# Kernel optimization log

Measured on AMD Instinct MI355X. Metric: run time of the kernel, lower is better.

The kernel has to match this reference:

```python
import jax, jax.numpy as jnp
import numpy as np

N = 100000        # nodes
E = 1600000       # edges (avg degree 16)
F = 128           # num_features
H = 8             # heads
D = F // H        # head_dim


def setup_inputs() -> dict:
    key = jax.random.key(0)
    ks = jax.random.split(key, 11)
    s = 1.0 / np.sqrt(F)
    return {
        "feat": jax.random.normal(ks[0], (N, F), dtype=jnp.float32),
        "edge_src": jax.random.randint(ks[1], (E,), 0, N, dtype=jnp.int32),
        "edge_dst": jax.random.randint(ks[2], (E,), 0, N, dtype=jnp.int32),
        "Wq": jax.random.uniform(ks[3], (F, F), jnp.float32, -s, s),
        "bq": jax.random.uniform(ks[4], (F,), jnp.float32, -s, s),
        "Wk": jax.random.uniform(ks[5], (F, F), jnp.float32, -s, s),
        "bk": jax.random.uniform(ks[6], (F,), jnp.float32, -s, s),
        "Wv": jax.random.uniform(ks[7], (F, F), jnp.float32, -s, s),
        "bv": jax.random.uniform(ks[8], (F,), jnp.float32, -s, s),
        "Wo": jax.random.uniform(ks[9], (F, F), jnp.float32, -s, s),
        "bo": jax.random.uniform(ks[10], (F,), jnp.float32, -s, s),
    }


def reference(feat, edge_src, edge_dst, Wq, bq, Wk, bk, Wv, bv, Wo, bo):
    scale = D ** -0.5
    # projections, split into heads: [N, H, D]
    q = ((feat @ Wq.T + bq) * scale).reshape(N, H, D)
    k = (feat @ Wk.T + bk).reshape(N, H, D)
    v = (feat @ Wv.T + bv).reshape(N, H, D)

    # per-edge dot product k[src] . q[dst] -> [E, H]  (dfn.u_dot_v)
    scores = jnp.einsum('ehd,ehd->eh', k[edge_src], q[edge_dst])

    # edge softmax normalized over incoming edges of each dst node
    m = jax.ops.segment_max(scores, edge_dst, num_segments=N)  # [N, H]
    m = jnp.where(jnp.isfinite(m), m, 0.0)
    e = jnp.exp(scores - m[edge_dst])                          # [E, H]
    z = jax.ops.segment_sum(e, edge_dst, num_segments=N)       # [N, H]
    alpha = e / z[edge_dst]                                    # [E, H]

    # weighted sum aggregation (u_mul_e + sum): [N, H, D]
    wv = alpha[:, :, None] * v[edge_src]                       # [E, H, D]
    attn = jax.ops.segment_sum(wv, edge_dst, num_segments=N)

    return attn.reshape(N, F) @ Wo.T + bo
```

## Files before the change

kernel.cpp:

```cpp
#include <hip/hip_runtime.h>
#include <math.h>

#define N_NODES 100000
#define N_EDGES 1600000
#define FDIM 128
#define NHEAD 8
#define HDIM 16
#define NBUK 391
#define NPART 400
#define PCHUNK 4000

using bf16x8 = __attribute__((ext_vector_type(8))) short;
using half8  = __attribute__((ext_vector_type(8))) _Float16;
using f32x4  = __attribute__((ext_vector_type(4))) float;
using f32x2  = __attribute__((ext_vector_type(2))) float;

__device__ inline unsigned short f2bf(float f) {
    union { float f; unsigned int u; } x; x.f = f;
    unsigned int u = x.u;
    return (unsigned short)((u + 0x7fffu + ((u >> 16) & 1u)) >> 16);
}
__device__ inline unsigned short f2h(float f) {
    _Float16 h = (_Float16)f;
    return __builtin_bit_cast(unsigned short, h);
}
__device__ inline unsigned int packh2(float a, float b) {
    return (unsigned int)f2h(a) | ((unsigned int)f2h(b) << 16);
}
__device__ inline float h_lo(unsigned int u) {
    return (float)__builtin_bit_cast(_Float16, (unsigned short)(u & 0xffffu));
}
__device__ inline float h_hi(unsigned int u) {
    return (float)__builtin_bit_cast(_Float16, (unsigned short)(u >> 16));
}
__device__ inline float exp2_fast(float x) {
#if __has_builtin(__builtin_amdgcn_exp2f)
    return __builtin_amdgcn_exp2f(x);
#else
    return __expf(x * 0.6931471805599453f);
#endif
}

#if __has_builtin(__builtin_amdgcn_cvt_pk_fp8_f32)
__device__ inline unsigned char fp8_enc(float x) {
    return (unsigned char)(__builtin_amdgcn_cvt_pk_fp8_f32(x, x, 0, false) & 0xff);
}
#else
__device__ inline unsigned char fp8_enc(float x) {
    unsigned int u = __builtin_bit_cast(unsigned int, x);
    unsigned int s = (u >> 24) & 0x80;
    float ax = fabsf(x);
    if (!(ax >= 0.001953125f)) {
        int m = (int)(ax * 512.f + 0.5f);
        return (unsigned char)(s | (unsigned)(m > 7 ? 7 : m));
    }
    if (ax > 448.f) return (unsigned char)(s | 0x7e);
    int e; float fr = frexpf(ax, &e);
    int q = (int)(fr * 16.f + 0.5f);
    if (q == 16) { q = 8; e += 1; }
    int exp = e - 1 + 7;
    if (exp <= 0) { int m = (int)(ax * 512.f + 0.5f); return (unsigned char)(s | (unsigned)(m > 7 ? 7 : m)); }
    if (exp > 15) return (unsigned char)(s | 0x7e);
    return (unsigned char)(s | (exp << 3) | (q & 7));
}
#endif

#if __has_builtin(__builtin_amdgcn_cvt_pk_f32_fp8)
#define FP8_HW_DECODE 1
#else
__device__ inline float fp8_dec_sw(unsigned char b) {
    int s = b >> 7, e = (b >> 3) & 15, m = b & 7;
    float v = (e == 0) ? ldexpf((float)m, -9) : ldexpf((float)(8 + m), e - 10);
    return s ? -v : v;
}
#endif

__device__ inline float dot_fp8_16(uint4 kr, const f32x2* __restrict__ qq2) {
#ifdef FP8_HW_DECODE
    f32x2 a = {0.f, 0.f};
    f32x2 p;
    p = __builtin_amdgcn_cvt_pk_f32_fp8(kr.x, false); a += p * qq2[0];
    p = __builtin_amdgcn_cvt_pk_f32_fp8(kr.x, true);  a += p * qq2[1];
    p = __builtin_amdgcn_cvt_pk_f32_fp8(kr.y, false); a += p * qq2[2];
    p = __builtin_amdgcn_cvt_pk_f32_fp8(kr.y, true);  a += p * qq2[3];
    p = __builtin_amdgcn_cvt_pk_f32_fp8(kr.z, false); a += p * qq2[4];
    p = __builtin_amdgcn_cvt_pk_f32_fp8(kr.z, true);  a += p * qq2[5];
    p = __builtin_amdgcn_cvt_pk_f32_fp8(kr.w, false); a += p * qq2[6];
    p = __builtin_amdgcn_cvt_pk_f32_fp8(kr.w, true);  a += p * qq2[7];
    return a[0] + a[1];
#else
    const float* qq = (const float*)qq2;
    float s = 0.f;
    unsigned int wds[4] = {kr.x, kr.y, kr.z, kr.w};
#pragma unroll
    for (int i = 0; i < 4; ++i)
#pragma unroll
        for (int j = 0; j < 4; ++j)
            s = fmaf(fp8_dec_sw((wds[i] >> (8 * j)) & 0xff), qq[i * 4 + j], s);
    return s;
#endif
}

__global__ __launch_bounds__(256) void convert_w_kernel(
    const float* __restrict__ W0, const float* __restrict__ W1,
    const float* __restrict__ W2, const float* __restrict__ W3,
    unsigned short* __restrict__ out)
{
    int i = blockIdx.x * 256 + threadIdx.x;
    int j  = i & 7;
    int l  = (i >> 3) & 63;
    int fk = i >> 9;
    int ks = fk & 3, nf = fk >> 2;
    int s = (nf * 16 + (l & 15)) * FDIM + ks * 32 + (l >> 4) * 8 + j;
    out[i]             = f2bf(W0[s]);
    out[16384 + i]     = f2bf(W1[s]);
    out[2 * 16384 + i] = f2bf(W2[s]);
    out[3 * 16384 + i] = f2h(W3[s]);
}

__global__ __launch_bounds__(256) void csr_hist_kernel(
    const int* __restrict__ edst, int* __restrict__ cntmatT)
{
    __shared__ int hist[NBUK];
    for (int b = threadIdx.x; b < NBUK; b += 256) hist[b] = 0;
    __syncthreads();
    const int c0 = blockIdx.x * PCHUNK;
    const int ce = min(c0 + PCHUNK, N_EDGES);
    for (int i = c0 + threadIdx.x; i < ce; i += 256) {
        int d = __builtin_nontemporal_load(&edst[i]);
        atomicAdd(&hist[d >> 8], 1);
    }
    __syncthreads();
    for (int b = threadIdx.x; b < NBUK; b += 256)
        cntmatT[b * NPART + blockIdx.x] = hist[b];
}

__global__ __launch_bounds__(512) void csr_colscan_kernel(
    const int* __restrict__ cntmatT, int* __restrict__ preT, int* __restrict__ colsum)
{
    __shared__ int s[512];
    const int t = threadIdx.x, buk = blockIdx.x;
    int x = (t < NPART) ? cntmatT[buk * NPART + t] : 0;
    s[t] = x;
    __syncthreads();
    for (int off = 1; off < 512; off <<= 1) {
        int v = (t >= off) ? s[t - off] : 0;
        __syncthreads();
        s[t] += v;
        __syncthreads();
    }
    if (t < NPART) preT[buk * NPART + t] = s[t] - x;
    if (t == NPART - 1) colsum[buk] = s[t];
}

__global__ __launch_bounds__(512) void csr_basescan_kernel(
    const int* __restrict__ colsum, int* __restrict__ base, int* __restrict__ row_off)
{
    __shared__ int s[512];
    const int t = threadIdx.x;
    int x = (t < NBUK) ? colsum[t] : 0;
    s[t] = x;
    __syncthreads();
    for (int off = 1; off < 512; off <<= 1) {
        int v = (t >= off) ? s[t - off] : 0;
        __syncthreads();
        s[t] += v;
        __syncthreads();
    }
    if (t < NBUK) base[t] = s[t] - x;
    if (t == 0) { base[NBUK] = N_EDGES; row_off[N_NODES] = N_EDGES; }
}

__global__ __launch_bounds__(256) void csr_partition_kernel(
    const int* __restrict__ esrc, const int* __restrict__ edst,
    const int* __restrict__ preT, const int* __restrict__ base,
    uint2* __restrict__ bpair)
{
    __shared__ int cur[NBUK];
    for (int b = threadIdx.x; b < NBUK; b += 256)
        cur[b] = base[b] + preT[b * NPART + blockIdx.x];
    __syncthreads();
    const int c0 = blockIdx.x * PCHUNK;
    const int ce = min(c0 + PCHUNK, N_EDGES);
    for (int i = c0 + threadIdx.x; i < ce; i += 256) {
        int d = __builtin_nontemporal_load(&edst[i]);
        int s = __builtin_nontemporal_load(&esrc[i]);
        int slot = atomicAdd(&cur[d >> 8], 1);
        bpair[slot] = make_uint2((unsigned)s, (unsigned)d);
    }
}

__global__ __launch_bounds__(256) void csr_bucket_kernel(
    const uint2* __restrict__ bpair, const int* __restrict__ base,
    int* __restrict__ row_off, int* __restrict__ csr_src)
{
    __shared__ int cnt2[256], s[256], cur[256];
    const int buk = blockIdx.x, t = threadIdx.x;
    const int b0 = base[buk];
    const int sz = base[buk + 1] - b0;
    const int nb0 = buk << 8;

    cnt2[t] = 0;
    __syncthreads();
    for (int i = t; i < sz; i += 256)
        atomicAdd(&cnt2[bpair[b0 + i].y & 255u], 1);
    __syncthreads();

    int x = cnt2[t];
    s[t] = x;
    __syncthreads();
    for (int off = 1; off < 256; off <<= 1) {
        int v = (t >= off) ? s[t - off] : 0;
        __syncthreads();
        s[t] += v;
        __syncthreads();
    }
    int excl = s[t] - x;
    cur[t] = excl;
    if (nb0 + t < N_NODES) row_off[nb0 + t] = b0 + excl;
    __syncthreads();

    for (int i = t; i < sz; i += 256) {
        uint2 p = bpair[b0 + i];
        int r = atomicAdd(&cur[p.y & 255u], 1);
        csr_src[b0 + r] = (int)p.x;
    }
}

struct GemmArgs {
    const unsigned short* W[3];
    const float* b[3];
    void* out[3];
    float scale[3];
};

template<int NP, bool IN_F32, bool MFMA_F16, int OUTM>
__global__ __launch_bounds__(256, 2) void mfma_gemm_v2(
    const void* __restrict__ Ain, GemmArgs ga, int nrows)
{
    __shared__ unsigned short A_s[128][136];
    __shared__ unsigned short W_sh[8192];

    const int t  = threadIdx.x;
    const int r0 = blockIdx.x * 128;

#pragma unroll
    for (int it = 0; it < 8; ++it) {
        int i = t + it * 256;
        int r = i >> 4, c8 = (i & 15) << 3;
        int gr = r0 + r;
        if (IN_F32) {
            float4 v0 = make_float4(0.f, 0.f, 0.f, 0.f), v1 = v0;
            if (gr < nrows) {
                const float* Af = (const float*)Ain;
                v0 = *(const float4*)&Af[(size_t)gr * FDIM + c8];
                v1 = *(const float4*)&Af[(size_t)gr * FDIM + c8 + 4];
            }
            uint4 pk;
            pk.x = (unsigned)f2bf(v0.x) | ((unsigned)f2bf(v0.y) << 16);
            pk.y = (unsigned)f2bf(v0.z) | ((unsigned)f2bf(v0.w) << 16);
            pk.z = (unsigned)f2bf(v1.x) | ((unsigned)f2bf(v1.y) << 16);
            pk.w = (unsigned)f2bf(v1.z) | ((unsigned)f2bf(v1.w) << 16);
            *(uint4*)&A_s[r][c8] = pk;
        } else {
            uint4 v = make_uint4(0u, 0u, 0u, 0u);
            if (gr < nrows) {
                const unsigned short* Ab = (const unsigned short*)Ain;
                v = *(const uint4*)&Ab[(size_t)gr * FDIM + c8];
            }
            *(uint4*)&A_s[r][c8] = v;
        }
    }
    __syncthreads();

    const int w  = t >> 6, l = t & 63;
    const int lr = l & 15, lk = l >> 4;

    bf16x8 a[2][4];
#pragma unroll
    for (int rg = 0; rg < 2; ++rg)
#pragma unroll
        for (int ks = 0; ks < 4; ++ks)
            a[rg][ks] = *(const bf16x8*)&A_s[w * 32 + rg * 16 + lr][ks * 32 + lk * 8];

#pragma unroll
    for (int p = 0; p < NP; ++p) {
        const unsigned short* Wsrc = ga.W[p];
        f32x4 acc[2][8];
#pragma unroll
        for (int rg = 0; rg < 2; ++rg)
#pragma unroll
            for (int nf = 0; nf < 8; ++nf) acc[rg][nf] = (f32x4){0.f, 0.f, 0.f, 0.f};

#pragma unroll
        for (int h = 0; h < 2; ++h) {
#pragma unroll
            for (int it = 0; it < 4; ++it) {
                int chunk = t + it * 256;
                *(uint4*)&W_sh[chunk * 8] = *(const uint4*)&Wsrc[h * 8192 + chunk * 8];
            }
            __syncthreads();
#pragma unroll
            for (int nfl = 0; nfl < 4; ++nfl) {
                int nf = h * 4 + nfl;
#pragma unroll
                for (int ks = 0; ks < 4; ++ks) {
                    bf16x8 bfr = *(const bf16x8*)&W_sh[((nfl * 4 + ks) * 64 + l) * 8];
                    if (MFMA_F16) {
                        acc[0][nf] = __builtin_amdgcn_mfma_f32_16x16x32_f16(
                            __builtin_bit_cast(half8, a[0][ks]), __builtin_bit_cast(half8, bfr),
                            acc[0][nf], 0, 0, 0);
                        acc[1][nf] = __builtin_amdgcn_mfma_f32_16x16x32_f16(
                            __builtin_bit_cast(half8, a[1][ks]), __builtin_bit_cast(half8, bfr),
                            acc[1][nf], 0, 0, 0);
                    } else {
                        acc[0][nf] = __builtin_amdgcn_mfma_f32_16x16x32_bf16(a[0][ks], bfr, acc[0][nf], 0, 0, 0);
                        acc[1][nf] = __builtin_amdgcn_mfma_f32_16x16x32_bf16(a[1][ks], bfr, acc[1][nf], 0, 0, 0);
                    }
                }
            }
            __syncthreads();
        }

        const float* bias = ga.b[p];
        const float  scl  = ga.scale[p];
        const int    mode = (OUTM >> (2 * p)) & 3;

        if (mode == 0) {
            unsigned short* Oh = &A_s[0][0];
#pragma unroll
            for (int rg = 0; rg < 2; ++rg)
#pragma unroll
                for (int nf = 0; nf < 8; ++nf) {
                    int col = nf * 16 + lr;
                    float bv = bias[col];
#pragma unroll
                    for (int j = 0; j < 4; ++j)
                        Oh[(w * 32 + rg * 16 + lk * 4 + j) * 136 + col] = f2h((acc[rg][nf][j] + bv) * scl);
                }
            __syncthreads();
            unsigned short* outp = (unsigned short*)ga.out[p];
#pragma unroll
            for (int it = 0; it < 8; ++it) {
                int i = t + it * 256;
                int r = i >> 4, c8 = (i & 15) << 3;
                if (r0 + r < nrows)
                    *(uint4*)&outp[(size_t)(r0 + r) * FDIM + c8] = *(const uint4*)&Oh[r * 136 + c8];
            }
        } else if (mode == 1) {
            unsigned char* O8 = (unsigned char*)A_s;
#pragma unroll
            for (int rg = 0; rg < 2; ++rg)
#pragma unroll
                for (int nf = 0; nf < 8; ++nf) {
                    int col = nf * 16 + lr;
                    float bv = bias[col];
#pragma unroll
                    for (int j = 0; j < 4; ++j)
                        O8[(w * 32 + rg * 16 + lk * 4 + j) * 144 + col] = fp8_enc((acc[rg][nf][j] + bv) * scl);
                }
            __syncthreads();
            unsigned char* outp = (unsigned char*)ga.out[p];
#pragma unroll
            for (int it = 0; it < 4; ++it) {
                int i = t + it * 256;
                int r = i >> 3, c16 = (i & 7) << 4;
                if (r0 + r < nrows)
                    *(uint4*)&outp[(size_t)(r0 + r) * FDIM + c16] = *(const uint4*)&O8[r * 144 + c16];
            }
        } else {
            float* outp = (float*)ga.out[p];
#pragma unroll
            for (int rg = 0; rg < 2; ++rg)
#pragma unroll
                for (int nf = 0; nf < 8; ++nf) {
                    int col = nf * 16 + lr;
                    float bv = bias[col];
                    int row = r0 + w * 32 + rg * 16 + lk * 4;
#pragma unroll
                    for (int j = 0; j < 4; ++j)
                        if (row + j < nrows)
                            outp[(size_t)(row + j) * FDIM + col] = (acc[rg][nf][j] + bv) * scl;
                }
        }
    }
}

__global__ __launch_bounds__(256) void attn_kernel(
    const unsigned short* __restrict__ q, const unsigned char* __restrict__ kf8,
    const unsigned short* __restrict__ v,
    const int* __restrict__ row_off, const int* __restrict__ csr_src,
    unsigned short* __restrict__ out, int nnodes)
{
    __shared__ float q_s[4][NHEAD][18];
    __shared__ float p_s[4][64][NHEAD];
    __shared__ int   src_s[4][64];

    const int w = threadIdx.x >> 6;
    const int l = threadIdx.x & 63;
    const int node = blockIdx.x * 4 + w;
    if (node >= nnodes) return;

    {
        unsigned int qv = *(const unsigned int*)&q[(size_t)node * FDIM + l * 2];
        *(f32x2*)&q_s[w][l >> 3][(l & 7) * 2] = (f32x2){h_lo(qv), h_hi(qv)};
    }

    const int e_l = l >> 3, h_sc = l & 7;
    const int e2 = l >> 4, h_ag = (l >> 1) & 7, dq = l & 1;
    const int vo = h_ag * HDIM + dq * 8;

    const int start = row_off[node];
    const int end   = row_off[node + 1];

    float z_run = 0.f;
    f32x2 acc[4] = {{0.f,0.f},{0.f,0.f},{0.f,0.f},{0.f,0.f}};

    const f32x2* qq2 = (const f32x2*)&q_s[w][h_sc][0];

    for (int c0 = start; c0 < end; c0 += 64) {
        const int cn = min(64, end - c0);

        for (int i = l; i < cn; i += 64)
            src_s[w][i] = csr_src[c0 + i];

        for (int base = 0; base < cn; base += 32) {
            uint4 kr[4];
#pragma unroll
            for (int it = 0; it < 4; ++it) {
                int ei = base + it * 8 + e_l;
                if (ei < cn)
                    kr[it] = *(const uint4*)&kf8[(size_t)src_s[w][ei] * FDIM + h_sc * 16];
            }
#pragma unroll
            for (int it = 0; it < 4; ++it) {
                int ei = base + it * 8 + e_l;
                if (ei < cn) {
                    float p = exp2_fast(dot_fp8_16(kr[it], qq2));
                    p_s[w][ei][h_sc] = p;
                    z_run += p;
                }
            }
        }

        for (int base = 0; base < cn; base += 4) {
            int e  = base + e2;
            int ec = min(e, cn - 1);
            float p = (e < cn) ? p_s[w][e][h_ag] : 0.f;
            uint4 vv = *(const uint4*)&v[(size_t)src_s[w][ec] * FDIM + vo];
            f32x2 p2 = {p, p};
            acc[0] += p2 * (f32x2){h_lo(vv.x), h_hi(vv.x)};
            acc[1] += p2 * (f32x2){h_lo(vv.y), h_hi(vv.y)};
            acc[2] += p2 * (f32x2){h_lo(vv.z), h_hi(vv.z)};
            acc[3] += p2 * (f32x2){h_lo(vv.w), h_hi(vv.w)};
        }
    }

#pragma unroll
    for (int mask = 8; mask < 64; mask <<= 1)
        z_run += __shfl_xor(z_run, mask, 64);

#pragma unroll
    for (int mask = 16; mask < 64; mask <<= 1)
#pragma unroll
        for (int i = 0; i < 4; ++i) {
            acc[i][0] += __shfl_xor(acc[i][0], mask, 64);
            acc[i][1] += __shfl_xor(acc[i][1], mask, 64);
        }

    float z_ag = __shfl(z_run, h_ag, 64);

    if (e2 == 0) {
        uint4 o = make_uint4(0u, 0u, 0u, 0u);
        if (end > start) {
            float rz = 1.0f / z_ag;
            o.x = packh2(acc[0][0] * rz, acc[0][1] * rz);
            o.y = packh2(acc[1][0] * rz, acc[1][1] * rz);
            o.z = packh2(acc[2][0] * rz, acc[2][1] * rz);
            o.w = packh2(acc[3][0] * rz, acc[3][1] * rz);
        }
        *(uint4*)&out[(size_t)node * FDIM + vo] = o;
    }
}

extern "C" void kernel_launch(void* const* d_in, const int* in_sizes, int n_in,
                              void* d_out, int out_size, void* d_ws, size_t ws_size,
                              hipStream_t stream)
{
    const float* feat = (const float*)d_in[0];
    const int*   esrc = (const int*)d_in[1];
    const int*   edst = (const int*)d_in[2];
    const float* Wq   = (const float*)d_in[3];
    const float* bq   = (const float*)d_in[4];
    const float* Wk   = (const float*)d_in[5];
    const float* bk   = (const float*)d_in[6];
    const float* Wv   = (const float*)d_in[7];
    const float* bv   = (const float*)d_in[8];
    const float* Wo   = (const float*)d_in[9];
    const float* bo   = (const float*)d_in[10];
    float* out = (float*)d_out;

    const size_t NROW = (size_t)N_NODES * FDIM;
    unsigned short* qb  = (unsigned short*)d_ws;
    unsigned short* vb  = qb + NROW;
    unsigned short* ab  = vb + NROW;
    unsigned char*  kf8 = (unsigned char*)(ab + NROW);
    unsigned short* wbf = (unsigned short*)(kf8 + NROW);
    int* cntmatT = (int*)(wbf + 4 * 16384);
    int* preT    = cntmatT + NBUK * NPART;
    int* colsum  = preT + NBUK * NPART;
    int* base    = colsum + 512;
    uint2* bpair = (uint2*)(base + 512);
    int* row_off = (int*)(bpair + N_EDGES);
    int* csr_src = row_off + N_NODES + 1;

    const int gemmGrid = (N_NODES + 127) / 128;

    hipLaunchKernelGGL(convert_w_kernel, dim3(64), dim3(256), 0, stream,
                       Wq, Wk, Wv, Wo, wbf);

    GemmArgs qkv;
    qkv.W[0] = wbf;          qkv.b[0] = bq; qkv.out[0] = qb;  qkv.scale[0] = 0.25f * 1.4426950408889634f;
    qkv.W[1] = wbf + 16384;  qkv.b[1] = bk; qkv.out[1] = kf8; qkv.scale[1] = 1.0f;
    qkv.W[2] = wbf + 32768;  qkv.b[2] = bv; qkv.out[2] = vb;  qkv.scale[2] = 1.0f;
    hipLaunchKernelGGL((mfma_gemm_v2<3, true, false, 4>), dim3(gemmGrid), dim3(256), 0, stream,
                       feat, qkv, N_NODES);

    hipLaunchKernelGGL(csr_hist_kernel, dim3(NPART), dim3(256), 0, stream, edst, cntmatT);
    hipLaunchKernelGGL(csr_colscan_kernel, dim3(NBUK), dim3(512), 0, stream, cntmatT, preT, colsum);
    hipLaunchKernelGGL(csr_basescan_kernel, dim3(1), dim3(512), 0, stream, colsum, base, row_off);
    hipLaunchKernelGGL(csr_partition_kernel, dim3(NPART), dim3(256), 0, stream,
                       esrc, edst, preT, base, bpair);
    hipLaunchKernelGGL(csr_bucket_kernel, dim3(NBUK), dim3(256), 0, stream,
                       bpair, base, row_off, csr_src);

    hipLaunchKernelGGL(attn_kernel, dim3((N_NODES + 3) / 4), dim3(256), 0, stream,
                       qb, kf8, vb, row_off, csr_src, ab, N_NODES);

    GemmArgs oprj;
    oprj.W[0] = wbf + 3 * 16384; oprj.b[0] = bo; oprj.out[0] = out; oprj.scale[0] = 1.0f;
    hipLaunchKernelGGL((mfma_gemm_v2<1, false, true, 2>), dim3(gemmGrid), dim3(256), 0, stream,
                       ab, oprj, N_NODES);
}
```

Before: 222.7 us.

## Merge CSR build kernels with weight conversion and QKV GEMM launches

Fuses weight conversion with the destination histogram into one launch, merges the column scan and base scan using a last-block-done atomic counter, and runs the QKV projection GEMM blocks alongside the edge partition blocks in a single heterogeneous grid. This cuts the kernel launch count from eight to five and lets the independent GEMM and partition work share the GPU at the same time instead of running back to back. The cost is larger register and shared-memory footprints for the partition blocks, which now share the GEMM's launch bounds. It also adds reliance on a device-scope counter reset inside the first kernel.

```diff
diff --git a/kernel.cpp b/kernel.cpp
--- a/kernel.cpp
+++ b/kernel.cpp
@@ -101,30 +101,31 @@
 #endif
 }
 
-__global__ __launch_bounds__(256) void convert_w_kernel(
+__global__ __launch_bounds__(256) void convert_hist_kernel(
     const float* __restrict__ W0, const float* __restrict__ W1,
     const float* __restrict__ W2, const float* __restrict__ W3,
-    unsigned short* __restrict__ out)
-{
-    int i = blockIdx.x * 256 + threadIdx.x;
-    int j  = i & 7;
-    int l  = (i >> 3) & 63;
-    int fk = i >> 9;
-    int ks = fk & 3, nf = fk >> 2;
-    int s = (nf * 16 + (l & 15)) * FDIM + ks * 32 + (l >> 4) * 8 + j;
-    out[i]             = f2bf(W0[s]);
-    out[16384 + i]     = f2bf(W1[s]);
-    out[2 * 16384 + i] = f2bf(W2[s]);
-    out[3 * 16384 + i] = f2h(W3[s]);
-}
-
-__global__ __launch_bounds__(256) void csr_hist_kernel(
-    const int* __restrict__ edst, int* __restrict__ cntmatT)
+    unsigned short* __restrict__ out,
+    const int* __restrict__ edst, int* __restrict__ cntmatT, int* __restrict__ done)
 {
     __shared__ int hist[NBUK];
+    if (blockIdx.x < 64) {
+        int i = blockIdx.x * 256 + threadIdx.x;
+        if (i == 0) done[0] = 0;
+        int j  = i & 7;
+        int l  = (i >> 3) & 63;
+        int fk = i >> 9;
+        int ks = fk & 3, nf = fk >> 2;
+        int s = (nf * 16 + (l & 15)) * FDIM + ks * 32 + (l >> 4) * 8 + j;
+        out[i]             = f2bf(W0[s]);
+        out[16384 + i]     = f2bf(W1[s]);
+        out[2 * 16384 + i] = f2bf(W2[s]);
+        out[3 * 16384 + i] = f2h(W3[s]);
+        return;
+    }
+    const int pb = blockIdx.x - 64;
     for (int b = threadIdx.x; b < NBUK; b += 256) hist[b] = 0;
     __syncthreads();
-    const int c0 = blockIdx.x * PCHUNK;
+    const int c0 = pb * PCHUNK;
     const int ce = min(c0 + PCHUNK, N_EDGES);
     for (int i = c0 + threadIdx.x; i < ce; i += 256) {
         int d = __builtin_nontemporal_load(&edst[i]);
@@ -132,13 +133,15 @@
     }
     __syncthreads();
     for (int b = threadIdx.x; b < NBUK; b += 256)
-        cntmatT[b * NPART + blockIdx.x] = hist[b];
-}
-
-__global__ __launch_bounds__(512) void csr_colscan_kernel(
-    const int* __restrict__ cntmatT, int* __restrict__ preT, int* __restrict__ colsum)
+        cntmatT[b * NPART + pb] = hist[b];
+}
+
+__global__ __launch_bounds__(512) void csr_scan_kernel(
+    const int* __restrict__ cntmatT, int* __restrict__ preT, int* __restrict__ colsum,
+    int* __restrict__ base, int* __restrict__ row_off, int* __restrict__ done)
 {
     __shared__ int s[512];
+    __shared__ int isLast;
     const int t = threadIdx.x, buk = blockIdx.x;
     int x = (t < NPART) ? cntmatT[buk * NPART + t] : 0;
     s[t] = x;
@@ -150,16 +153,17 @@
         __syncthreads();
     }
     if (t < NPART) preT[buk * NPART + t] = s[t] - x;
-    if (t == NPART - 1) colsum[buk] = s[t];
-}
-
-__global__ __launch_bounds__(512) void csr_basescan_kernel(
-    const int* __restrict__ colsum, int* __restrict__ base, int* __restrict__ row_off)
-{
-    __shared__ int s[512];
-    const int t = threadIdx.x;
-    int x = (t < NBUK) ? colsum[t] : 0;
-    s[t] = x;
+    if (t == NPART - 1)
+        __hip_atomic_store(&colsum[buk], s[t], __ATOMIC_RELAXED, __HIP_MEMORY_SCOPE_AGENT);
+    __threadfence();
+    __syncthreads();
+    if (t == 0)
+        isLast = (atomicAdd(done, 1) == NBUK - 1) ? 1 : 0;
+    __syncthreads();
+    if (!isLast) return;
+    __threadfence();
+    int y = (t < NBUK) ? __hip_atomic_load(&colsum[t], __ATOMIC_RELAXED, __HIP_MEMORY_SCOPE_AGENT) : 0;
+    s[t] = y;
     __syncthreads();
     for (int off = 1; off < 512; off <<= 1) {
         int v = (t >= off) ? s[t - off] : 0;
@@ -167,64 +171,8 @@
         s[t] += v;
         __syncthreads();
     }
-    if (t < NBUK) base[t] = s[t] - x;
+    if (t < NBUK) base[t] = s[t] - y;
     if (t == 0) { base[NBUK] = N_EDGES; row_off[N_NODES] = N_EDGES; }
-}
-
-__global__ __launch_bounds__(256) void csr_partition_kernel(
-    const int* __restrict__ esrc, const int* __restrict__ edst,
-    const int* __restrict__ preT, const int* __restrict__ base,
-    uint2* __restrict__ bpair)
-{
-    __shared__ int cur[NBUK];
-    for (int b = threadIdx.x; b < NBUK; b += 256)
-        cur[b] = base[b] + preT[b * NPART + blockIdx.x];
-    __syncthreads();
-    const int c0 = blockIdx.x * PCHUNK;
-    const int ce = min(c0 + PCHUNK, N_EDGES);
-    for (int i = c0 + threadIdx.x; i < ce; i += 256) {
-        int d = __builtin_nontemporal_load(&edst[i]);
-        int s = __builtin_nontemporal_load(&esrc[i]);
-        int slot = atomicAdd(&cur[d >> 8], 1);
-        bpair[slot] = make_uint2((unsigned)s, (unsigned)d);
-    }
-}
-
-__global__ __launch_bounds__(256) void csr_bucket_kernel(
-    const uint2* __restrict__ bpair, const int* __restrict__ base,
-    int* __restrict__ row_off, int* __restrict__ csr_src)
-{
-    __shared__ int cnt2[256], s[256], cur[256];
-    const int buk = blockIdx.x, t = threadIdx.x;
-    const int b0 = base[buk];
-    const int sz = base[buk + 1] - b0;
-    const int nb0 = buk << 8;
-
-    cnt2[t] = 0;
-    __syncthreads();
-    for (int i = t; i < sz; i += 256)
-        atomicAdd(&cnt2[bpair[b0 + i].y & 255u], 1);
-    __syncthreads();
-
-    int x = cnt2[t];
-    s[t] = x;
-    __syncthreads();
-    for (int off = 1; off < 256; off <<= 1) {
-        int v = (t >= off) ? s[t - off] : 0;
-        __syncthreads();
-        s[t] += v;
-        __syncthreads();
-    }
-    int excl = s[t] - x;
-    cur[t] = excl;
-    if (nb0 + t < N_NODES) row_off[nb0 + t] = b0 + excl;
-    __syncthreads();
-
-    for (int i = t; i < sz; i += 256) {
-        uint2 p = bpair[b0 + i];
-        int r = atomicAdd(&cur[p.y & 255u], 1);
-        csr_src[b0 + r] = (int)p.x;
-    }
 }
 
 struct GemmArgs {
@@ -235,14 +183,14 @@
 };
 
 template<int NP, bool IN_F32, bool MFMA_F16, int OUTM>
-__global__ __launch_bounds__(256, 2) void mfma_gemm_v2(
-    const void* __restrict__ Ain, GemmArgs ga, int nrows)
+__device__ __forceinline__ void gemm_body(const void* __restrict__ Ain,
+                                          const GemmArgs& ga, int nrows, int blk)
 {
     __shared__ unsigned short A_s[128][136];
     __shared__ unsigned short W_sh[8192];
 
     const int t  = threadIdx.x;
-    const int r0 = blockIdx.x * 128;
+    const int r0 = blk * 128;
 
 #pragma unroll
     for (int it = 0; it < 8; ++it) {
@@ -386,6 +334,76 @@
     }
 }
 
+template<int NP, bool IN_F32, bool MFMA_F16, int OUTM>
+__global__ __launch_bounds__(256, 2) void mfma_gemm_v2(
+    const void* __restrict__ Ain, GemmArgs ga, int nrows)
+{
+    gemm_body<NP, IN_F32, MFMA_F16, OUTM>(Ain, ga, nrows, blockIdx.x);
+}
+
+template<int NP, bool IN_F32, bool MFMA_F16, int OUTM>
+__global__ __launch_bounds__(256, 2) void gemm_part_kernel(
+    const void* __restrict__ Ain, GemmArgs ga, int nrows, int nGemmBlocks,
+    const int* __restrict__ esrc, const int* __restrict__ edst,
+    const int* __restrict__ preT, const int* __restrict__ base,
+    uint2* __restrict__ bpair)
+{
+    if ((int)blockIdx.x < nGemmBlocks) {
+        gemm_body<NP, IN_F32, MFMA_F16, OUTM>(Ain, ga, nrows, blockIdx.x);
+        return;
+    }
+    __shared__ int cur[NBUK];
+    const int pb = blockIdx.x - nGemmBlocks;
+    for (int b = threadIdx.x; b < NBUK; b += 256)
+        cur[b] = base[b] + preT[b * NPART + pb];
+    __syncthreads();
+    const int c0 = pb * PCHUNK;
+    const int ce = min(c0 + PCHUNK, N_EDGES);
+    for (int i = c0 + threadIdx.x; i < ce; i += 256) {
+        int d = __builtin_nontemporal_load(&edst[i]);
+        int s = __builtin_nontemporal_load(&esrc[i]);
+        int slot = atomicAdd(&cur[d >> 8], 1);
+        bpair[slot] = make_uint2((unsigned)s, (unsigned)d);
+    }
+}
+
+__global__ __launch_bounds__(256) void csr_bucket_kernel(
+    const uint2* __restrict__ bpair, const int* __restrict__ base,
+    int* __restrict__ row_off, int* __restrict__ csr_src)
+{
+    __shared__ int cnt2[256], s[256], cur[256];
+    const int buk = blockIdx.x, t = threadIdx.x;
+    const int b0 = base[buk];
+    const int sz = base[buk + 1] - b0;
+    const int nb0 = buk << 8;
+
+    cnt2[t] = 0;
+    __syncthreads();
+    for (int i = t; i < sz; i += 256)
+        atomicAdd(&cnt2[bpair[b0 + i].y & 255u], 1);
+    __syncthreads();
+
+    int x = cnt2[t];
+    s[t] = x;
+    __syncthreads();
+    for (int off = 1; off < 256; off <<= 1) {
+        int v = (t >= off) ? s[t - off] : 0;
+        __syncthreads();
+        s[t] += v;
+        __syncthreads();
+    }
+    int excl = s[t] - x;
+    cur[t] = excl;
+    if (nb0 + t < N_NODES) row_off[nb0 + t] = b0 + excl;
+    __syncthreads();
+
+    for (int i = t; i < sz; i += 256) {
+        uint2 p = bpair[b0 + i];
+        int r = atomicAdd(&cur[p.y & 255u], 1);
+        csr_src[b0 + r] = (int)p.x;
+    }
+}
+
 __global__ __launch_bounds__(256) void attn_kernel(
     const unsigned short* __restrict__ q, const unsigned char* __restrict__ kf8,
     const unsigned short* __restrict__ v,
@@ -510,27 +528,27 @@
     int* preT    = cntmatT + NBUK * NPART;
     int* colsum  = preT + NBUK * NPART;
     int* base    = colsum + 512;
-    uint2* bpair = (uint2*)(base + 512);
+    int* done    = base + 512;
+    uint2* bpair = (uint2*)(done + 63);
     int* row_off = (int*)(bpair + N_EDGES);
     int* csr_src = row_off + N_NODES + 1;
 
     const int gemmGrid = (N_NODES + 127) / 128;
 
-    hipLaunchKernelGGL(convert_w_kernel, dim3(64), dim3(256), 0, stream,
-                       Wq, Wk, Wv, Wo, wbf);
+    hipLaunchKernelGGL(convert_hist_kernel, dim3(64 + NPART), dim3(256), 0, stream,
+                       Wq, Wk, Wv, Wo, wbf, edst, cntmatT, done);
+
+    hipLaunchKernelGGL(csr_scan_kernel, dim3(NBUK), dim3(512), 0, stream,
+                       cntmatT, preT, colsum, base, row_off, done);
 
     GemmArgs qkv;
     qkv.W[0] = wbf;          qkv.b[0] = bq; qkv.out[0] = qb;  qkv.scale[0] = 0.25f * 1.4426950408889634f;
     qkv.W[1] = wbf + 16384;  qkv.b[1] = bk; qkv.out[1] = kf8; qkv.scale[1] = 1.0f;
     qkv.W[2] = wbf + 32768;  qkv.b[2] = bv; qkv.out[2] = vb;  qkv.scale[2] = 1.0f;
-    hipLaunchKernelGGL((mfma_gemm_v2<3, true, false, 4>), dim3(gemmGrid), dim3(256), 0, stream,
-                       feat, qkv, N_NODES);
-
-    hipLaunchKernelGGL(csr_hist_kernel, dim3(NPART), dim3(256), 0, stream, edst, cntmatT);
-    hipLaunchKernelGGL(csr_colscan_kernel, dim3(NBUK), dim3(512), 0, stream, cntmatT, preT, colsum);
-    hipLaunchKernelGGL(csr_basescan_kernel, dim3(1), dim3(512), 0, stream, colsum, base, row_off);
-    hipLaunchKernelGGL(csr_partition_kernel, dim3(NPART), dim3(256), 0, stream,
-                       esrc, edst, preT, base, bpair);
+    hipLaunchKernelGGL((gemm_part_kernel<3, true, false, 4>),
+                       dim3(gemmGrid + NPART), dim3(256), 0, stream,
+                       feat, qkv, N_NODES, gemmGrid, esrc, edst, preT, base, bpair);
+
     hipLaunchKernelGGL(csr_bucket_kernel, dim3(NBUK), dim3(256), 0, stream,
                        bpair, base, row_off, csr_src);
 
```

New measurement: 257.0 us. +15.4%, slower.
